# Kernel optimization log

Hardware: AMD Instinct MI355X
Metric: run time of the kernel (lower is better)

The kernel has to match this reference:

```python
import jax, jax.numpy as jnp
import numpy as np

B, S, H, R, DEPTH = 64, 32, 1024, 256, 9  # batch, seq, hidden, GRU hidden (h//reduction), tree depth


def _gru(x, h, W_ih, W_hh, b_ih, b_hh):
    # PyTorch nn.GRUCell math
    gi = x @ W_ih.T + b_ih
    gh = h @ W_hh.T + b_hh
    i_r, i_z, i_n = jnp.split(gi, 3, axis=-1)
    h_r, h_z, h_n = jnp.split(gh, 3, axis=-1)
    r = jax.nn.sigmoid(i_r + h_r)
    z = jax.nn.sigmoid(i_z + h_z)
    n = jnp.tanh(i_n + r * h_n)
    return (1.0 - z) * n + z * h


def _forward(x, W_hidden, b_hidden, W_hb, b_hb, W_branch, b_branch, W_ih, W_hh, b_ih, b_hh, tree_depth):
    selu = jax.nn.selu
    # root: discretize(selu(hidden(selu(x)))).mean over sequence; discretize=identity (discretize kw None)
    xc = selu(selu(x) @ W_hidden.T + b_hidden).mean(axis=1)[:, None, :]  # [B,1,H]
    hc = jnp.zeros((x.shape[0], 1, W_hh.shape[1]), x.dtype)              # [B,1,R]
    depth = jnp.zeros((x.shape[0], 1, 1), x.dtype)
    for _ in range(tree_depth):  # level-synchronous expansion of the recursive generate()
        hc = _gru(xc, hc, W_ih, W_hh, b_ih, b_hh)
        xh = jnp.concatenate([xc, hc], axis=-1)                          # [B,N,H+R]
        hb = jax.nn.sigmoid(xh @ W_hb.T + b_hb)                          # [B,N,1]
        depth = depth + hb
        lr = selu(xh @ W_branch.T + b_branch)                            # [B,N,2H]
        l, r = jnp.split(lr, 2, axis=-1)
        l = xc - selu(l @ W_hidden.T + b_hidden)                          # residual left child
        r = xc - selu(r @ W_hidden.T + b_hidden)                          # residual right child
        Bn, N, Hd = xc.shape
        xc = jnp.stack([l, r], axis=2).reshape(Bn, 2 * N, Hd)
        hc = jnp.repeat(hc, 2, axis=1)
        depth = jnp.repeat(depth, 2, axis=1)
    # leaf nodes: final controller step; terminal = x (no V head), depth += has_branches
    hc = _gru(xc, hc, W_ih, W_hh, b_ih, b_hh)
    hb = jax.nn.sigmoid(jnp.concatenate([xc, hc], axis=-1) @ W_hb.T + b_hb)
    depth = depth + hb
    return jnp.concatenate([xc, depth], axis=-1)  # [B, 2**D, H+1]: leaf terminals + leaf depths


def setup_inputs() -> dict:
    key = jax.random.key(0)
    ks = jax.random.split(key, 6)
    def w(k, o, i):
        return (jax.random.normal(k, (o, i), jnp.float32) / np.sqrt(i)).astype(jnp.float32)
    return {
        'x': jax.random.normal(ks[0], (B, S, H), jnp.float32),
        'W_hidden': w(ks[1], H, H), 'b_hidden': jnp.zeros((H,), jnp.float32),
        'W_hb': w(ks[2], 1, H + R), 'b_hb': jnp.zeros((1,), jnp.float32),
        'W_branch': w(ks[3], 2 * H, H + R), 'b_branch': jnp.zeros((2 * H,), jnp.float32),
        'W_ih': w(ks[4], 3 * R, H), 'W_hh': w(ks[5], 3 * R, R),
        'b_ih': jnp.zeros((3 * R,), jnp.float32), 'b_hh': jnp.zeros((3 * R,), jnp.float32),
        'tree_depth': DEPTH,
    }


def reference(x, W_hidden, b_hidden, W_hb, b_hb, W_branch, b_branch, W_ih, W_hh, b_ih, b_hh, tree_depth):
    return _forward(x, W_hidden, b_hidden, W_hb, b_hb, W_branch, b_branch, W_ih, W_hh, b_ih, b_hh, tree_depth)
```

## Files before the change

### kernel.cpp

```cpp
#include <hip/hip_runtime.h>
#include <hip/hip_bf16.h>
#include <cstdint>
#include <cstddef>


#define SELU_L 1.0507009873554805f
#define SELU_A 1.6732632423543772f

__device__ __forceinline__ float selu_f(float x) {
    return x > 0.f ? SELU_L * x : (SELU_L * SELU_A) * (__expf(x) - 1.f);
}
__device__ __forceinline__ float sigmoid_f(float x) {
    return 1.f / (1.f + __expf(-x));
}

typedef __attribute__((ext_vector_type(8))) short s16x8;
typedef __attribute__((ext_vector_type(4))) float f32x4;

__device__ __forceinline__ void gld16(const void* g, void* l) {
    __builtin_amdgcn_global_load_lds(
        (const __attribute__((address_space(1))) uint32_t*)g,
        (__attribute__((address_space(3))) uint32_t*)l, 16, 0, 0);
}

enum { AM_PLAIN = 0, AM_CONCAT = 2 };
enum { EP_NONE = 0, EP_SELU32 = 1, EP_BRANCH = 2, EP_RESID = 3 };

template <int AMODE, int EPI>
__global__ __launch_bounds__(256) void mgemm(
    int M, int N, int K,
    const __hip_bfloat16* __restrict__ A, int lda,
    const __hip_bfloat16* __restrict__ A2,
    const __hip_bfloat16* __restrict__ W,
    const float* __restrict__ bias,
    void* __restrict__ Cv, int ldc,
    const __hip_bfloat16* __restrict__ P,
    float* __restrict__ C32, int ldc32)
{
    __shared__ short As[4096];
    __shared__ short Bs[4096];

    const int tid  = threadIdx.x;
    const int wave = tid >> 6;
    const int lane = tid & 63;

    int bxi = blockIdx.x, byi = blockIdx.y;
    {
        const int ncol = gridDim.x, nrow = gridDim.y;
        if ((nrow & 7) == 0) {
            const int lin = byi * ncol + bxi;
            const int xcd = lin & 7;
            const int t = lin >> 3;
            const int rows_per = nrow >> 3;
            bxi = t % ncol;
            byi = xcd * rows_per + t / ncol;
        }
    }
    const int bm = byi * 128;
    const int bn = bxi * 128;

    const int s0 = wave * 128 + lane;
    const int s1 = s0 + 64;
    const int r0 = s0 >> 2, j0 = ((s0 & 3) - (r0 >> 1)) & 3;
    const int r1 = s1 >> 2, j1 = ((s1 & 3) - (r1 >> 1)) & 3;
    const int ga0 = min(bm + r0, M - 1);
    const int ga1 = min(bm + r1, M - 1);

    const short* gA0; const short* gA1;
    const short* gA0b = nullptr; const short* gA1b = nullptr;
    if (AMODE == AM_CONCAT) {
        gA0  = (const short*)A  + (size_t)ga0 * 1024 + j0 * 8;
        gA1  = (const short*)A  + (size_t)ga1 * 1024 + j1 * 8;
        gA0b = (const short*)A2 + (size_t)ga0 * 256  + j0 * 8;
        gA1b = (const short*)A2 + (size_t)ga1 * 256  + j1 * 8;
    } else {
        gA0 = (const short*)A + (size_t)ga0 * lda + j0 * 8;
        gA1 = (const short*)A + (size_t)ga1 * lda + j1 * 8;
    }
    const short* gB0 = (const short*)W + (size_t)(bn + r0) * K + j0 * 8;
    const short* gB1 = (const short*)W + (size_t)(bn + r1) * K + j1 * 8;

    short* dA0 = &As[wave * 1024];
    short* dA1 = &As[wave * 1024 + 512];
    short* dB0 = &Bs[wave * 1024];
    short* dB1 = &Bs[wave * 1024 + 512];

    const int wm = (wave >> 1) * 64, wn = (wave & 1) * 64;
    const int l16 = lane & 15, q4 = lane >> 4;
    int aoff[4], boff[4];
#pragma unroll
    for (int i = 0; i < 4; ++i) {
        int ra = wm + i * 16 + l16;
        aoff[i] = ra * 32 + (((q4 + (ra >> 1)) & 3) << 3);
        int rb = wn + i * 16 + l16;
        boff[i] = rb * 32 + (((q4 + (rb >> 1)) & 3) << 3);
    }

    f32x4 acc[4][4] = {};

    for (int k0 = 0; k0 < K; k0 += 32) {
        if (AMODE == AM_CONCAT) {
            const short* a0 = (k0 < 1024) ? gA0 + k0 : gA0b + (k0 - 1024);
            const short* a1 = (k0 < 1024) ? gA1 + k0 : gA1b + (k0 - 1024);
            gld16(a0, dA0);
            gld16(a1, dA1);
        } else {
            gld16(gA0 + k0, dA0);
            gld16(gA1 + k0, dA1);
        }
        gld16(gB0 + k0, dB0);
        gld16(gB1 + k0, dB1);
        __syncthreads();

        s16x8 af[4], bf[4];
#pragma unroll
        for (int i = 0; i < 4; ++i) af[i] = *(const s16x8*)&As[aoff[i]];
#pragma unroll
        for (int i = 0; i < 4; ++i) bf[i] = *(const s16x8*)&Bs[boff[i]];
#pragma unroll
        for (int mi = 0; mi < 4; ++mi)
#pragma unroll
            for (int ni = 0; ni < 4; ++ni)
                acc[mi][ni] = __builtin_amdgcn_mfma_f32_16x16x32_bf16(
                    af[mi], bf[ni], acc[mi][ni], 0, 0, 0);
        __syncthreads();
    }

    const int crow0 = bm + wm + q4 * 4;
    const int ccol0 = bn + wn + l16;
#pragma unroll
    for (int mi = 0; mi < 4; ++mi) {
#pragma unroll
        for (int r = 0; r < 4; ++r) {
            const int row = crow0 + mi * 16 + r;
            if (row >= M) continue;
#pragma unroll
            for (int ni = 0; ni < 4; ++ni) {
                const int col = ccol0 + ni * 16;
                float v = acc[mi][ni][r] + bias[col];
                if (EPI == EP_NONE) {
                    ((float*)Cv)[(size_t)row * ldc + col] = v;
                } else if (EPI == EP_SELU32) {
                    ((float*)Cv)[(size_t)row * ldc + col] = selu_f(v);
                } else if (EPI == EP_BRANCH) {
                    const int c = col >> 10, jj = col & 1023;
                    ((__hip_bfloat16*)Cv)[(size_t)(2 * row + c) * 1024 + jj] =
                        __float2bfloat16(selu_f(v));
                } else {
                    const float pv = __bfloat162float(P[(size_t)(row >> 1) * 1024 + col]);
                    const float o = pv - selu_f(v);
                    ((__hip_bfloat16*)Cv)[(size_t)row * 1024 + col] = __float2bfloat16(o);
                    if (C32) C32[(size_t)row * ldc32 + col] = o;
                }
            }
        }
    }
}

__global__ void cvt_bf16_k(const float* __restrict__ in, __hip_bfloat16* __restrict__ out, int n)
{
    int i = blockIdx.x * 256 + threadIdx.x;
    if (i < n) out[i] = __float2bfloat16(in[i]);
}

__global__ void selu_cvt_k(const float* __restrict__ in, __hip_bfloat16* __restrict__ out, int n)
{
    int i = blockIdx.x * 256 + threadIdx.x;
    if (i < n) out[i] = __float2bfloat16(selu_f(in[i]));
}

__global__ void mean_kernel(const float* __restrict__ T, __hip_bfloat16* __restrict__ xc)
{
    const int idx = blockIdx.x * 256 + threadIdx.x;
    const int b = idx >> 10, h = idx & 1023;
    const float* p = T + (size_t)b * 32 * 1024 + h;
    float s = 0.f;
#pragma unroll
    for (int si = 0; si < 32; ++si) s += p[si * 1024];
    xc[idx] = __float2bfloat16(s * (1.f / 32.f));
}

__global__ __launch_bounds__(256) void gateshb_kernel(
    const float* __restrict__ gi,
    const float* __restrict__ gh,
    const float* __restrict__ b_hh,
    const __hip_bfloat16* __restrict__ hold,
    __hip_bfloat16* __restrict__ hnew,
    const __hip_bfloat16* __restrict__ xc,
    const float* __restrict__ W_hb,
    const float* __restrict__ b_hb,
    const float* __restrict__ depth_old,
    float* __restrict__ depth_out, int dstride,
    int first)
{
    const int m = blockIdx.x;
    const int j = threadIdx.x;
    __shared__ float red[4];

    const float* gim = gi + (size_t)m * 768;
    const float ir = gim[j], iz = gim[256 + j], in_ = gim[512 + j];
    float hr, hz, hn, h0;
    if (first) {
        hr = b_hh[j]; hz = b_hh[256 + j]; hn = b_hh[512 + j]; h0 = 0.f;
    } else {
        const float* ghm = gh + (size_t)(m >> 1) * 768;
        hr = ghm[j]; hz = ghm[256 + j]; hn = ghm[512 + j];
        h0 = __bfloat162float(hold[(size_t)(m >> 1) * 256 + j]);
    }
    const float r = sigmoid_f(ir + hr);
    const float z = sigmoid_f(iz + hz);
    const float n = tanhf(in_ + r * hn);
    const float hv = (1.f - z) * n + z * h0;
    hnew[(size_t)m * 256 + j] = __float2bfloat16(hv);

    const __hip_bfloat16* xr = xc + (size_t)m * 1024;
    float s = hv * W_hb[1024 + j];
#pragma unroll
    for (int kk = 0; kk < 4; ++kk) {
        const int k = j + kk * 256;
        s += __bfloat162float(xr[k]) * W_hb[k];
    }
#pragma unroll
    for (int off = 32; off; off >>= 1) s += __shfl_down(s, off);
    if ((j & 63) == 0) red[j >> 6] = s;
    __syncthreads();
    if (j == 0) {
        const float tot = red[0] + red[1] + red[2] + red[3];
        const float hb = sigmoid_f(tot + b_hb[0]);
        const float d0 = first ? 0.f : depth_old[m >> 1];
        depth_out[(size_t)m * dstride] = d0 + hb;
    }
}

extern "C" void kernel_launch(void* const* d_in, const int* in_sizes, int n_in,
                              void* d_out, int out_size, void* d_ws, size_t ws_size,
                              hipStream_t stream)
{
    const float* x        = (const float*)d_in[0];
    const float* W_hidden = (const float*)d_in[1];
    const float* b_hidden = (const float*)d_in[2];
    const float* W_hb     = (const float*)d_in[3];
    const float* b_hb     = (const float*)d_in[4];
    const float* W_branch = (const float*)d_in[5];
    const float* b_branch = (const float*)d_in[6];
    const float* W_ih     = (const float*)d_in[7];
    const float* W_hh     = (const float*)d_in[8];
    const float* b_ih     = (const float*)d_in[9];
    const float* b_hh     = (const float*)d_in[10];

    char* ws = (char*)d_ws;
    size_t off = 0;
    auto alloc = [&](size_t bytes) {
        void* p = ws + off;
        off += (bytes + 255) & ~(size_t)255;
        return p;
    };
    __hip_bfloat16* Whb  = (__hip_bfloat16*)alloc(1024 * 1024 * 2);
    __hip_bfloat16* Wbb  = (__hip_bfloat16*)alloc(2048 * 1280 * 2);
    __hip_bfloat16* Wib  = (__hip_bfloat16*)alloc(768 * 1024 * 2);
    __hip_bfloat16* Whh  = (__hip_bfloat16*)alloc(768 * 256 * 2);
    __hip_bfloat16* Xs   = (__hip_bfloat16*)alloc((size_t)2048 * 1024 * 2);
    float*          GI   = (float*)alloc((size_t)32768 * 768 * 4);
    __hip_bfloat16* U    = (__hip_bfloat16*)alloc((size_t)32768 * 1024 * 2);
    __hip_bfloat16* XC0  = (__hip_bfloat16*)alloc((size_t)32768 * 1024 * 2);
    __hip_bfloat16* XC1  = (__hip_bfloat16*)alloc((size_t)32768 * 1024 * 2);
    __hip_bfloat16* HC0  = (__hip_bfloat16*)alloc((size_t)32768 * 256 * 2);
    __hip_bfloat16* HC1  = (__hip_bfloat16*)alloc((size_t)32768 * 256 * 2);
    float*          D0   = (float*)alloc(32768 * 4);
    float*          D1   = (float*)alloc(32768 * 4);
    float*          GH   = (float*)U;

    float* out = (float*)d_out;

    cvt_bf16_k<<<(1024 * 1024 + 255) / 256, 256, 0, stream>>>(W_hidden, Whb, 1024 * 1024);
    cvt_bf16_k<<<(2048 * 1280 + 255) / 256, 256, 0, stream>>>(W_branch, Wbb, 2048 * 1280);
    cvt_bf16_k<<<(768 * 1024 + 255) / 256, 256, 0, stream>>>(W_ih, Wib, 768 * 1024);
    cvt_bf16_k<<<(768 * 256 + 255) / 256, 256, 0, stream>>>(W_hh, Whh, 768 * 256);
    selu_cvt_k<<<(2048 * 1024 + 255) / 256, 256, 0, stream>>>(x, Xs, 2048 * 1024);

    mgemm<AM_PLAIN, EP_SELU32><<<dim3(1024 / 128, 2048 / 128), 256, 0, stream>>>(
        2048, 1024, 1024, Xs, 1024, nullptr, Whb, b_hidden, GI, 1024, nullptr, nullptr, 0);
    mean_kernel<<<(64 * 1024) / 256, 256, 0, stream>>>(GI, XC0);

    __hip_bfloat16* xc_cur = XC0; __hip_bfloat16* xc_next = XC1;
    __hip_bfloat16* hc_prev = nullptr; __hip_bfloat16* hc_new = HC0;
    float* d_prev = nullptr; float* d_next = D0;

    for (int d = 0; d < 9; ++d) {
        const int M = 64 << d;
        mgemm<AM_PLAIN, EP_NONE><<<dim3(768 / 128, (M + 127) / 128), 256, 0, stream>>>(
            M, 768, 1024, xc_cur, 1024, nullptr, Wib, b_ih, GI, 768, nullptr, nullptr, 0);
        if (d > 0) {
            mgemm<AM_PLAIN, EP_NONE><<<dim3(768 / 128, (M / 2 + 127) / 128), 256, 0, stream>>>(
                M / 2, 768, 256, hc_prev, 256, nullptr, Whh, b_hh, GH, 768, nullptr, nullptr, 0);
        }
        gateshb_kernel<<<M, 256, 0, stream>>>(
            GI, (const float*)GH, b_hh, hc_prev, hc_new,
            xc_cur, W_hb, b_hb, d_prev, d_next, 1, d == 0 ? 1 : 0);
        mgemm<AM_CONCAT, EP_BRANCH><<<dim3(2048 / 128, (M + 127) / 128), 256, 0, stream>>>(
            M, 2048, 1280, xc_cur, 1024, hc_new, Wbb, b_branch, U, 1024, nullptr, nullptr, 0);
        mgemm<AM_PLAIN, EP_RESID><<<dim3(1024 / 128, (2 * M) / 128), 256, 0, stream>>>(
            2 * M, 1024, 1024, U, 1024, nullptr, Whb, b_hidden, xc_next, 1024,
            xc_cur, d == 8 ? out : nullptr, 1025);

        __hip_bfloat16* t = xc_cur; xc_cur = xc_next; xc_next = t;
        hc_prev = hc_new; hc_new = (hc_new == HC0) ? HC1 : HC0;
        d_prev = d_next;  d_next = (d_next == D0) ? D1 : D0;
    }

    {
        const int M = 32768;
        mgemm<AM_PLAIN, EP_NONE><<<dim3(768 / 128, M / 128), 256, 0, stream>>>(
            M, 768, 1024, xc_cur, 1024, nullptr, Wib, b_ih, GI, 768, nullptr, nullptr, 0);
        mgemm<AM_PLAIN, EP_NONE><<<dim3(768 / 128, (M / 2) / 128), 256, 0, stream>>>(
            M / 2, 768, 256, hc_prev, 256, nullptr, Whh, b_hh, GH, 768, nullptr, nullptr, 0);
        gateshb_kernel<<<M, 256, 0, stream>>>(
            GI, (const float*)GH, b_hh, hc_prev, hc_new,
            xc_cur, W_hb, b_hb, d_prev, out + 1024, 1025, 0);
    }
}
```

Measured before the change: 1.720 ms.

## Double GEMM K-tile to 64, batch GI/GH GEMMs and weight conversions into single launches

The GEMM body now stages 64-wide K slices per barrier, using an 8-way swizzled LDS layout and two MFMA sub-steps, which halves the number of sync points and doubles LDS use to 32 KB per block. The input-gate and hidden-gate GEMMs of each level are merged into one launch split on blockIdx.z, and the four weight conversion kernels are merged into one. The aim is to cut barrier and launch overhead. In exchange, LDS pressure is higher, which may lower occupancy, and the paired launch has empty blocks for the smaller GEMM.

Result: faster. 1.489 ms (-13.5%).

```diff
diff --git a/kernel.cpp b/kernel.cpp
--- a/kernel.cpp
+++ b/kernel.cpp
@@ -27,63 +27,41 @@
 enum { EP_NONE = 0, EP_SELU32 = 1, EP_BRANCH = 2, EP_RESID = 3 };
 
 template <int AMODE, int EPI>
-__global__ __launch_bounds__(256) void mgemm(
-    int M, int N, int K,
+__device__ __forceinline__ void gemm_body(
+    int bm, int bn, int M, int K,
     const __hip_bfloat16* __restrict__ A, int lda,
     const __hip_bfloat16* __restrict__ A2,
     const __hip_bfloat16* __restrict__ W,
     const float* __restrict__ bias,
     void* __restrict__ Cv, int ldc,
     const __hip_bfloat16* __restrict__ P,
-    float* __restrict__ C32, int ldc32)
-{
-    __shared__ short As[4096];
-    __shared__ short Bs[4096];
-
+    float* __restrict__ C32, int ldc32,
+    short* As, short* Bs)
+{
     const int tid  = threadIdx.x;
     const int wave = tid >> 6;
     const int lane = tid & 63;
 
-    int bxi = blockIdx.x, byi = blockIdx.y;
-    {
-        const int ncol = gridDim.x, nrow = gridDim.y;
-        if ((nrow & 7) == 0) {
-            const int lin = byi * ncol + bxi;
-            const int xcd = lin & 7;
-            const int t = lin >> 3;
-            const int rows_per = nrow >> 3;
-            bxi = t % ncol;
-            byi = xcd * rows_per + t / ncol;
-        }
-    }
-    const int bm = byi * 128;
-    const int bn = bxi * 128;
-
-    const int s0 = wave * 128 + lane;
-    const int s1 = s0 + 64;
-    const int r0 = s0 >> 2, j0 = ((s0 & 3) - (r0 >> 1)) & 3;
-    const int r1 = s1 >> 2, j1 = ((s1 & 3) - (r1 >> 1)) & 3;
-    const int ga0 = min(bm + r0, M - 1);
-    const int ga1 = min(bm + r1, M - 1);
-
-    const short* gA0; const short* gA1;
-    const short* gA0b = nullptr; const short* gA1b = nullptr;
-    if (AMODE == AM_CONCAT) {
-        gA0  = (const short*)A  + (size_t)ga0 * 1024 + j0 * 8;
-        gA1  = (const short*)A  + (size_t)ga1 * 1024 + j1 * 8;
-        gA0b = (const short*)A2 + (size_t)ga0 * 256  + j0 * 8;
-        gA1b = (const short*)A2 + (size_t)ga1 * 256  + j1 * 8;
-    } else {
-        gA0 = (const short*)A + (size_t)ga0 * lda + j0 * 8;
-        gA1 = (const short*)A + (size_t)ga1 * lda + j1 * 8;
-    }
-    const short* gB0 = (const short*)W + (size_t)(bn + r0) * K + j0 * 8;
-    const short* gB1 = (const short*)W + (size_t)(bn + r1) * K + j1 * 8;
-
-    short* dA0 = &As[wave * 1024];
-    short* dA1 = &As[wave * 1024 + 512];
-    short* dB0 = &Bs[wave * 1024];
-    short* dB1 = &Bs[wave * 1024 + 512];
+    const short* gA[4]; const short* gA2p[4]; const short* gB[4];
+    short* dA[4]; short* dB[4];
+#pragma unroll
+    for (int r = 0; r < 4; ++r) {
+        const int s   = r * 256 + wave * 64 + lane;
+        const int row = s >> 3;
+        const int pc  = s & 7;
+        const int j   = (pc - (row >> 1)) & 7;
+        const int ga  = min(bm + row, M - 1);
+        if (AMODE == AM_CONCAT) {
+            gA[r]   = (const short*)A  + (size_t)ga * 1024 + j * 8;
+            gA2p[r] = (const short*)A2 + (size_t)ga * 256  + j * 8;
+        } else {
+            gA[r]   = (const short*)A + (size_t)ga * lda + j * 8;
+            gA2p[r] = nullptr;
+        }
+        gB[r] = (const short*)W + (size_t)(bn + row) * K + j * 8;
+        dA[r] = &As[(size_t)(r * 256 + wave * 64) * 8];
+        dB[r] = &Bs[(size_t)(r * 256 + wave * 64) * 8];
+    }
 
     const int wm = (wave >> 1) * 64, wn = (wave & 1) * 64;
     const int l16 = lane & 15, q4 = lane >> 4;
@@ -91,38 +69,41 @@
 #pragma unroll
     for (int i = 0; i < 4; ++i) {
         int ra = wm + i * 16 + l16;
-        aoff[i] = ra * 32 + (((q4 + (ra >> 1)) & 3) << 3);
+        aoff[i] = ra * 64 + (((q4 + (ra >> 1)) & 7) << 3);
         int rb = wn + i * 16 + l16;
-        boff[i] = rb * 32 + (((q4 + (rb >> 1)) & 3) << 3);
+        boff[i] = rb * 64 + (((q4 + (rb >> 1)) & 7) << 3);
     }
 
     f32x4 acc[4][4] = {};
 
-    for (int k0 = 0; k0 < K; k0 += 32) {
-        if (AMODE == AM_CONCAT) {
-            const short* a0 = (k0 < 1024) ? gA0 + k0 : gA0b + (k0 - 1024);
-            const short* a1 = (k0 < 1024) ? gA1 + k0 : gA1b + (k0 - 1024);
-            gld16(a0, dA0);
-            gld16(a1, dA1);
-        } else {
-            gld16(gA0 + k0, dA0);
-            gld16(gA1 + k0, dA1);
-        }
-        gld16(gB0 + k0, dB0);
-        gld16(gB1 + k0, dB1);
+    for (int k0 = 0; k0 < K; k0 += 64) {
+#pragma unroll
+        for (int r = 0; r < 4; ++r) {
+            const short* ap;
+            if (AMODE == AM_CONCAT)
+                ap = (k0 < 1024) ? gA[r] + k0 : gA2p[r] + (k0 - 1024);
+            else
+                ap = gA[r] + k0;
+            gld16(ap, dA[r]);
+            gld16(gB[r] + k0, dB[r]);
+        }
         __syncthreads();
 
-        s16x8 af[4], bf[4];
-#pragma unroll
-        for (int i = 0; i < 4; ++i) af[i] = *(const s16x8*)&As[aoff[i]];
-#pragma unroll
-        for (int i = 0; i < 4; ++i) bf[i] = *(const s16x8*)&Bs[boff[i]];
-#pragma unroll
-        for (int mi = 0; mi < 4; ++mi)
-#pragma unroll
-            for (int ni = 0; ni < 4; ++ni)
-                acc[mi][ni] = __builtin_amdgcn_mfma_f32_16x16x32_bf16(
-                    af[mi], bf[ni], acc[mi][ni], 0, 0, 0);
+#pragma unroll
+        for (int h = 0; h < 2; ++h) {
+            const int hx = h << 5;
+            s16x8 af[4], bf[4];
+#pragma unroll
+            for (int i = 0; i < 4; ++i) af[i] = *(const s16x8*)&As[aoff[i] ^ hx];
+#pragma unroll
+            for (int i = 0; i < 4; ++i) bf[i] = *(const s16x8*)&Bs[boff[i] ^ hx];
+#pragma unroll
+            for (int mi = 0; mi < 4; ++mi)
+#pragma unroll
+                for (int ni = 0; ni < 4; ++ni)
+                    acc[mi][ni] = __builtin_amdgcn_mfma_f32_16x16x32_bf16(
+                        af[mi], bf[ni], acc[mi][ni], 0, 0, 0);
+        }
         __syncthreads();
     }
 
@@ -157,10 +138,80 @@
     }
 }
 
-__global__ void cvt_bf16_k(const float* __restrict__ in, __hip_bfloat16* __restrict__ out, int n)
+template <int AMODE, int EPI>
+__global__ __launch_bounds__(256) void mgemm(
+    int M, int N, int K,
+    const __hip_bfloat16* __restrict__ A, int lda,
+    const __hip_bfloat16* __restrict__ A2,
+    const __hip_bfloat16* __restrict__ W,
+    const float* __restrict__ bias,
+    void* __restrict__ Cv, int ldc,
+    const __hip_bfloat16* __restrict__ P,
+    float* __restrict__ C32, int ldc32)
+{
+    __shared__ short As[8192];
+    __shared__ short Bs[8192];
+    int bxi = blockIdx.x, byi = blockIdx.y;
+    {
+        const int ncol = gridDim.x, nrow = gridDim.y;
+        if ((nrow & 7) == 0) {
+            const int lin = byi * ncol + bxi;
+            const int xcd = lin & 7;
+            const int t = lin >> 3;
+            const int rows_per = nrow >> 3;
+            bxi = t % ncol;
+            byi = xcd * rows_per + t / ncol;
+        }
+    }
+    gemm_body<AMODE, EPI>(byi * 128, bxi * 128, M, K, A, lda, A2, W, bias,
+                          Cv, ldc, P, C32, ldc32, As, Bs);
+}
+
+struct GPair {
+    int M0, K0; const __hip_bfloat16* A0; int lda0;
+    const __hip_bfloat16* W0; const float* b0; float* C0; int ldc0;
+    int M1, K1; const __hip_bfloat16* A1; int lda1;
+    const __hip_bfloat16* W1; const float* b1; float* C1; int ldc1;
+};
+__global__ __launch_bounds__(256) void mgemm_pair(GPair g)
+{
+    __shared__ short As[8192];
+    __shared__ short Bs[8192];
+    int bxi = blockIdx.x, byi = blockIdx.y;
+    if (blockIdx.z == 0) {
+        const int ncol = gridDim.x, nrow = gridDim.y;
+        if ((nrow & 7) == 0) {
+            const int lin = byi * ncol + bxi;
+            const int xcd = lin & 7;
+            const int t = lin >> 3;
+            const int rows_per = nrow >> 3;
+            bxi = t % ncol;
+            byi = xcd * rows_per + t / ncol;
+        }
+        gemm_body<AM_PLAIN, EP_NONE>(byi * 128, bxi * 128, g.M0, g.K0,
+                                     g.A0, g.lda0, nullptr, g.W0, g.b0,
+                                     g.C0, g.ldc0, nullptr, nullptr, 0, As, Bs);
+    } else {
+        if (byi * 128 >= g.M1) return;
+        gemm_body<AM_PLAIN, EP_NONE>(byi * 128, bxi * 128, g.M1, g.K1,
+                                     g.A1, g.lda1, nullptr, g.W1, g.b1,
+                                     g.C1, g.ldc1, nullptr, nullptr, 0, As, Bs);
+    }
+}
+
+__global__ void cvt4_k(const float* __restrict__ s0, __hip_bfloat16* __restrict__ d0, int n0,
+                       const float* __restrict__ s1, __hip_bfloat16* __restrict__ d1, int n1,
+                       const float* __restrict__ s2, __hip_bfloat16* __restrict__ d2, int n2,
+                       const float* __restrict__ s3, __hip_bfloat16* __restrict__ d3, int n3)
 {
     int i = blockIdx.x * 256 + threadIdx.x;
-    if (i < n) out[i] = __float2bfloat16(in[i]);
+    if (i < n0) { d0[i] = __float2bfloat16(s0[i]); return; }
+    i -= n0;
+    if (i < n1) { d1[i] = __float2bfloat16(s1[i]); return; }
+    i -= n1;
+    if (i < n2) { d2[i] = __float2bfloat16(s2[i]); return; }
+    i -= n2;
+    if (i < n3) { d3[i] = __float2bfloat16(s3[i]); }
 }
 
 __global__ void selu_cvt_k(const float* __restrict__ in, __hip_bfloat16* __restrict__ out, int n)
@@ -272,10 +323,11 @@
 
     float* out = (float*)d_out;
 
-    cvt_bf16_k<<<(1024 * 1024 + 255) / 256, 256, 0, stream>>>(W_hidden, Whb, 1024 * 1024);
-    cvt_bf16_k<<<(2048 * 1280 + 255) / 256, 256, 0, stream>>>(W_branch, Wbb, 2048 * 1280);
-    cvt_bf16_k<<<(768 * 1024 + 255) / 256, 256, 0, stream>>>(W_ih, Wib, 768 * 1024);
-    cvt_bf16_k<<<(768 * 256 + 255) / 256, 256, 0, stream>>>(W_hh, Whh, 768 * 256);
+    {
+        const int n0 = 1024 * 1024, n1 = 2048 * 1280, n2 = 768 * 1024, n3 = 768 * 256;
+        cvt4_k<<<(n0 + n1 + n2 + n3 + 255) / 256, 256, 0, stream>>>(
+            W_hidden, Whb, n0, W_branch, Wbb, n1, W_ih, Wib, n2, W_hh, Whh, n3);
+    }
     selu_cvt_k<<<(2048 * 1024 + 255) / 256, 256, 0, stream>>>(x, Xs, 2048 * 1024);
 
     mgemm<AM_PLAIN, EP_SELU32><<<dim3(1024 / 128, 2048 / 128), 256, 0, stream>>>(
@@ -288,12 +340,13 @@
 
     for (int d = 0; d < 9; ++d) {
         const int M = 64 << d;
-        mgemm<AM_PLAIN, EP_NONE><<<dim3(768 / 128, (M + 127) / 128), 256, 0, stream>>>(
-            M, 768, 1024, xc_cur, 1024, nullptr, Wib, b_ih, GI, 768, nullptr, nullptr, 0);
-        if (d > 0) {
-            mgemm<AM_PLAIN, EP_NONE><<<dim3(768 / 128, (M / 2 + 127) / 128), 256, 0, stream>>>(
-                M / 2, 768, 256, hc_prev, 256, nullptr, Whh, b_hh, GH, 768, nullptr, nullptr, 0);
-        }
+        GPair g;
+        g.M0 = M;     g.K0 = 1024; g.A0 = xc_cur;  g.lda0 = 1024;
+        g.W0 = Wib;   g.b0 = b_ih; g.C0 = GI;      g.ldc0 = 768;
+        g.M1 = M / 2; g.K1 = 256;  g.A1 = hc_prev; g.lda1 = 256;
+        g.W1 = Whh;   g.b1 = b_hh; g.C1 = GH;      g.ldc1 = 768;
+        mgemm_pair<<<dim3(768 / 128, (M + 127) / 128, d > 0 ? 2 : 1), 256, 0, stream>>>(g);
+
         gateshb_kernel<<<M, 256, 0, stream>>>(
             GI, (const float*)GH, b_hh, hc_prev, hc_new,
             xc_cur, W_hb, b_hb, d_prev, d_next, 1, d == 0 ? 1 : 0);
@@ -310,10 +363,12 @@
 
     {
         const int M = 32768;
-        mgemm<AM_PLAIN, EP_NONE><<<dim3(768 / 128, M / 128), 256, 0, stream>>>(
-            M, 768, 1024, xc_cur, 1024, nullptr, Wib, b_ih, GI, 768, nullptr, nullptr, 0);
-        mgemm<AM_PLAIN, EP_NONE><<<dim3(768 / 128, (M / 2) / 128), 256, 0, stream>>>(
-            M / 2, 768, 256, hc_prev, 256, nullptr, Whh, b_hh, GH, 768, nullptr, nullptr, 0);
+        GPair g;
+        g.M0 = M;     g.K0 = 1024; g.A0 = xc_cur;  g.lda0 = 1024;
+        g.W0 = Wib;   g.b0 = b_ih; g.C0 = GI;      g.ldc0 = 768;
+        g.M1 = M / 2; g.K1 = 256;  g.A1 = hc_prev; g.lda1 = 256;
+        g.W1 = Whh;   g.b1 = b_hh; g.C1 = GH;      g.ldc1 = 768;
+        mgemm_pair<<<dim3(768 / 128, M / 128, 2), 256, 0, stream>>>(g);
         gateshb_kernel<<<M, 256, 0, stream>>>(
             GI, (const float*)GH, b_hh, hc_prev, hc_new,
             xc_cur, W_hb, b_hb, d_prev, out + 1024, 1025, 0);
```
